# Kernel tuning notes

Measured on AMD Instinct MI355X. Metric: run time of the kernel, lower is better.

The kernel has to match this reference:

```python
import jax, jax.numpy as jnp
import numpy as np

N = 20000      # nodes (single node type)
E = 320000     # edges per relation (avg degree 16)
R = 3          # relations / edge types
L = 3          # layers
H = 4          # heads
D = 64         # dim per head (hid_size // n_heads)
IN = 256       # in_size == hid_size
OUT = 128      # out_size
NEG_SLOPE = 0.2


def setup_inputs() -> dict:
    key = jax.random.key(0)
    ks = jax.random.split(key, 8)
    x = jax.random.normal(ks[0], (N, IN), jnp.float32)
    edge_src = jax.random.randint(ks[1], (R, E), 0, N, dtype=jnp.int32)
    edge_dst = jax.random.randint(ks[2], (R, E), 0, N, dtype=jnp.int32)
    W = jax.random.normal(ks[3], (L, R, IN, H * D), jnp.float32) * (1.0 / np.sqrt(IN))
    attn_l = jax.random.normal(ks[4], (L, R, H, D), jnp.float32) * 0.1
    attn_r = jax.random.normal(ks[5], (L, R, H, D), jnp.float32) * 0.1
    bias = jnp.zeros((L, R, H * D), jnp.float32)
    fc_w = jax.random.normal(ks[6], (IN, OUT), jnp.float32) * (1.0 / np.sqrt(IN))
    fc_b = jnp.zeros((OUT,), jnp.float32)
    return dict(x=x, edge_src=edge_src, edge_dst=edge_dst, W=W,
                attn_l=attn_l, attn_r=attn_r, bias=bias, fc_w=fc_w, fc_b=fc_b)


def _gat_conv(h, src, dst, W_r, al, ar, b_r):
    # h: [N, IN] -> feat: [N, H, D]
    feat = (h @ W_r).reshape(N, H, D)
    el = jnp.sum(feat * al, axis=-1)                      # [N, H]
    er = jnp.sum(feat * ar, axis=-1)                      # [N, H]
    e = jax.nn.leaky_relu(el[src] + er[dst], NEG_SLOPE)   # [E, H]
    # segment softmax over incoming edges of each dst node, per head
    m = jax.ops.segment_max(e, dst, num_segments=N)       # [N, H]
    a = jnp.exp(e - m[dst])
    s = jax.ops.segment_sum(a, dst, num_segments=N)       # [N, H]
    alpha = a / s[dst]                                    # [E, H]
    # weighted scatter-add of source features: [N, H, D]
    out = jax.ops.segment_sum(alpha[:, :, None] * feat[src], dst, num_segments=N)
    return out + b_r.reshape(1, H, D)


def reference(x, edge_src, edge_dst, W, attn_l, attn_r, bias, fc_w, fc_b):
    h = x
    for l in range(L):
        acc = jnp.zeros((N, H, D), h.dtype)
        for r in range(R):  # sum-aggregate across relations (HeteroGraphConv aggregate='sum')
            acc = acc + _gat_conv(h, edge_src[r], edge_dst[r],
                                  W[l, r], attn_l[l, r], attn_r[l, r], bias[l, r])
        h = acc.reshape(N, H * D)
        if l != L - 1:
            h = jax.nn.relu(h)  # dropout = identity in eval
    return h @ fc_w + fc_b  # [N, OUT]
```

## Files before the change

kernel.cpp:

```cpp
#include <hip/hip_runtime.h>
#include <math.h>

#define NN 20000
#define NN_PAD 20096
#define EE 320000
#define RR 3
#define LL 3
#define HH 4
#define DD 64
#define CDIM 256
#define OUTD 128
#define NEG 0.2f

typedef float f32x4 __attribute__((ext_vector_type(4)));
typedef short sh8 __attribute__((ext_vector_type(8)));

__device__ __forceinline__ ushort f2bf(float f) {
    union { float f; uint u; } v; v.f = f;
    uint r = (v.u + 0x7FFF + ((v.u >> 16) & 1)) >> 16;
    return (ushort)r;
}
__device__ __forceinline__ float bf2f(ushort u) {
    union { uint u; float f; } v; v.u = ((uint)u) << 16;
    return v.f;
}
__device__ __forceinline__ float bflo(uint p) { return bf2f((ushort)(p & 0xffff)); }
__device__ __forceinline__ float bfhi(uint p) { return bf2f((ushort)(p >> 16)); }

__device__ __forceinline__ void glds16(const ushort* g, ushort* l) {
    __builtin_amdgcn_global_load_lds(
        (const __attribute__((address_space(1))) void*)g,
        (__attribute__((address_space(3))) void*)l, 16, 0, 0);
}


__global__ void count_deg(const int* __restrict__ edge_dst, int* __restrict__ deg) {
    int i = blockIdx.x * blockDim.x + threadIdx.x;
    if (i >= RR * EE) return;
    int r = i / EE;
    atomicAdd(&deg[r * NN + edge_dst[i]], 1);
}

__global__ __launch_bounds__(1024) void scan_kernel(
    const int* __restrict__ deg, int* __restrict__ row_ptr, int* __restrict__ cursor) {
    int r = blockIdx.x;
    const int* d = deg + r * NN;
    int* rp = row_ptr + r * (NN + 1);
    int* cur = cursor + r * (NN + 1);
    __shared__ int wsum[16];
    int lane = threadIdx.x & 63, wv = threadIdx.x >> 6;
    if (threadIdx.x == 0) { rp[0] = 0; cur[0] = 0; }
    int carry = 0;
    for (int base = 0; base < NN; base += 1024) {
        int i = base + threadIdx.x;
        int v = (i < NN) ? d[i] : 0;
        int s = v;
        #pragma unroll
        for (int off = 1; off < 64; off <<= 1) {
            int n = __shfl_up(s, off, 64);
            if (lane >= off) s += n;
        }
        if (lane == 63) wsum[wv] = s;
        __syncthreads();
        if (wv == 0) {
            int ws = (lane < 16) ? wsum[lane] : 0;
            #pragma unroll
            for (int off = 1; off < 16; off <<= 1) {
                int n = __shfl_up(ws, off, 64);
                if (lane >= off) ws += n;
            }
            if (lane < 16) wsum[lane] = ws;
        }
        __syncthreads();
        int incl = carry + (wv ? wsum[wv - 1] : 0) + s;
        if (i < NN) { rp[i + 1] = incl; cur[i + 1] = incl; }
        carry += wsum[15];
        __syncthreads();
    }
}

__global__ void fill_csr(const int* __restrict__ edge_src, const int* __restrict__ edge_dst,
                         int* __restrict__ cursor, int* __restrict__ csr_src) {
    int i = blockIdx.x * blockDim.x + threadIdx.x;
    if (i >= RR * EE) return;
    int r = i / EE;
    int dst = edge_dst[i];
    int pos = atomicAdd(&cursor[r * (NN + 1) + dst], 1);
    csr_src[r * EE + pos] = edge_src[i];
}


__global__ void cvt_bf16x4(const float* __restrict__ in, ushort* __restrict__ out, int n4) {
    int i = blockIdx.x * blockDim.x + threadIdx.x;
    if (i >= n4) return;
    float4 v = *(const float4*)(in + (size_t)i * 4);
    ushort4 o;
    o.x = f2bf(v.x); o.y = f2bf(v.y); o.z = f2bf(v.z); o.w = f2bf(v.w);
    *(ushort4*)(out + (size_t)i * 4) = o;
}

__global__ void prep_all(const float* __restrict__ W, const float* __restrict__ fc_w,
                         ushort* __restrict__ Wt, ushort* __restrict__ fct) {
    __shared__ float tile[32][33];
    int z = blockIdx.z;
    const float* src;
    ushort* dst;
    int N;
    if (z < LL * RR) {
        src = W + (size_t)z * CDIM * CDIM;
        dst = Wt + (size_t)z * CDIM * CDIM;
        N = CDIM;
    } else {
        src = fc_w;
        dst = fct;
        N = OUTD;
    }
    int kb = blockIdx.x * 32, nb = blockIdx.y * 32;
    if (nb >= N) return;
    for (int yy = threadIdx.y; yy < 32; yy += 8)
        tile[yy][threadIdx.x] = src[(size_t)(kb + yy) * N + nb + threadIdx.x];
    __syncthreads();
    for (int yy = threadIdx.y; yy < 32; yy += 8)
        dst[(size_t)(nb + yy) * CDIM + kb + threadIdx.x] = f2bf(tile[threadIdx.x][yy]);
}


#define TM 128
#define TN 128
#define TK 32

__global__ __launch_bounds__(256) void gemm_bf16(
    const ushort* __restrict__ A, const ushort* __restrict__ Bt0, void* __restrict__ C0,
    int M, int K, int Ncol, long strideB, long strideC,
    const float* __restrict__ bias, int out_fp32,
    const float* __restrict__ al_all, const float* __restrict__ ar_all,
    float* __restrict__ el_all, float* __restrict__ er_all) {
    __shared__ alignas(16) ushort As[TM * 32];
    __shared__ alignas(16) ushort Bs[TN * 32];
    const ushort* Bt = Bt0 + (size_t)blockIdx.z * strideB;
    int m0 = blockIdx.x * TM, n0 = blockIdx.y * TN;
    int t = threadIdx.x;
    int wave = t >> 6, lane = t & 63;
    int q = lane >> 4, l16 = lane & 15;
    int wrow = (wave >> 1) * 64, wcol = (wave & 1) * 64;

    int sw = (q ^ ((l16 >> 1) & 3)) * 8;
    int a_off[4], b_off[4];
    #pragma unroll
    for (int i = 0; i < 4; i++) {
        a_off[i] = (wrow + i * 16 + l16) * 32 + sw;
        b_off[i] = (wcol + i * 16 + l16) * 32 + sw;
    }
    int row_a = t >> 2;
    int ch_a  = ((t & 3) ^ ((row_a >> 1) & 3)) * 8;

    f32x4 acc[4][4];
    #pragma unroll
    for (int i = 0; i < 4; i++)
        #pragma unroll
        for (int j = 0; j < 4; j++)
            #pragma unroll
            for (int k = 0; k < 4; k++) acc[i][j][k] = 0.f;

    for (int k0 = 0; k0 < K; k0 += TK) {
        #pragma unroll
        for (int s = 0; s < 2; s++) {
            int qid = t + s * 256;
            int row = row_a + s * 64;
            glds16(A + (size_t)(m0 + row) * K + k0 + ch_a, As + qid * 8);
        }
        #pragma unroll
        for (int s = 0; s < 2; s++) {
            int qid = t + s * 256;
            int row = row_a + s * 64;
            glds16(Bt + (size_t)(n0 + row) * K + k0 + ch_a, Bs + qid * 8);
        }
        __syncthreads();
        sh8 af[4], bfr[4];
        #pragma unroll
        for (int i = 0; i < 4; i++) af[i] = *(const sh8*)(As + a_off[i]);
        #pragma unroll
        for (int j = 0; j < 4; j++) bfr[j] = *(const sh8*)(Bs + b_off[j]);
        #pragma unroll
        for (int i = 0; i < 4; i++)
            #pragma unroll
            for (int j = 0; j < 4; j++)
                acc[i][j] = __builtin_amdgcn_mfma_f32_16x16x32_bf16(af[i], bfr[j], acc[i][j], 0, 0, 0);
        __syncthreads();
    }

    if (out_fp32) {
        float* C = (float*)C0 + (size_t)blockIdx.z * strideC;
        #pragma unroll
        for (int i = 0; i < 4; i++) {
            #pragma unroll
            for (int reg = 0; reg < 4; reg++) {
                int row = m0 + wrow + i * 16 + q * 4 + reg;
                if (row >= M) continue;
                #pragma unroll
                for (int j = 0; j < 4; j++) {
                    int col = n0 + wcol + j * 16 + l16;
                    float v = acc[i][j][reg];
                    if (bias) v += bias[col];
                    C[(size_t)row * Ncol + col] = v;
                }
            }
        }
    } else {
        ushort* C = (ushort*)C0 + (size_t)blockIdx.z * strideC;
        #pragma unroll
        for (int i = 0; i < 4; i++) {
            #pragma unroll
            for (int reg = 0; reg < 4; reg++) {
                int row = m0 + wrow + i * 16 + q * 4 + reg;
                if (row >= M) continue;
                #pragma unroll
                for (int j = 0; j < 4; j++) {
                    int col = n0 + wcol + j * 16 + l16;
                    C[(size_t)row * Ncol + col] = f2bf(acc[i][j][reg]);
                }
            }
        }
    }

    if (el_all) {
        const float* al = al_all + (size_t)blockIdx.z * CDIM;
        const float* ar = ar_all + (size_t)blockIdx.z * CDIM;
        float* elp = el_all + (size_t)blockIdx.z * NN * HH;
        float* erp = er_all + (size_t)blockIdx.z * NN * HH;
        int head = (n0 + wcol) >> 6;
        float alj[4], arj[4];
        #pragma unroll
        for (int j = 0; j < 4; j++) {
            int gcol = n0 + wcol + j * 16 + l16;
            alj[j] = al[gcol];
            arj[j] = ar[gcol];
        }
        #pragma unroll
        for (int i = 0; i < 4; i++) {
            #pragma unroll
            for (int reg = 0; reg < 4; reg++) {
                int row = m0 + wrow + i * 16 + q * 4 + reg;
                float pl = 0.f, pr = 0.f;
                #pragma unroll
                for (int j = 0; j < 4; j++) {
                    pl = fmaf(acc[i][j][reg], alj[j], pl);
                    pr = fmaf(acc[i][j][reg], arj[j], pr);
                }
                #pragma unroll
                for (int m = 1; m < 16; m <<= 1) {
                    pl += __shfl_xor(pl, m, 64);
                    pr += __shfl_xor(pr, m, 64);
                }
                if (l16 == 0 && row < M) {
                    elp[(size_t)row * HH + head] = pl;
                    erp[(size_t)row * HH + head] = pr;
                }
            }
        }
    }
}

__global__ __launch_bounds__(256) void aggregate_fused(
    const ushort* __restrict__ feat16, const float* __restrict__ el,
    const float* __restrict__ er, const int* __restrict__ row_ptr,
    const int* __restrict__ csr_src, const float* __restrict__ bias,
    ushort* __restrict__ hout, int relu) {
    int wv = threadIdx.x >> 6, lane = threadIdx.x & 63;
    int node = blockIdx.x * 4 + wv;
    if (node >= NN) return;
    int c0 = lane * 4;
    int h = lane >> 4;
    float t0 = 0.f, t1 = 0.f, t2 = 0.f, t3 = 0.f;
    #pragma unroll
    for (int r = 0; r < RR; r++) {
        const int* rp = row_ptr + r * (NN + 1);
        int beg = rp[node], end = rp[node + 1];
        const ushort* fr = feat16 + (size_t)r * NN * CDIM;
        const float* elr = el + (size_t)r * NN * HH;
        float ern = er[((size_t)r * NN + node) * HH + h];
        const int* cs = csr_src + (size_t)r * EE;
        float p0 = 0.f, p1 = 0.f, p2 = 0.f, p3 = 0.f, ssum = 0.f;
        int e = beg;
        for (; e + 4 <= end; e += 4) {
            int s0 = cs[e], s1 = cs[e + 1], s2 = cs[e + 2], s3 = cs[e + 3];
            float x0 = elr[s0 * HH + h];
            float x1 = elr[s1 * HH + h];
            float x2 = elr[s2 * HH + h];
            float x3 = elr[s3 * HH + h];
            uint2 f0 = *(const uint2*)(fr + (size_t)s0 * CDIM + c0);
            uint2 f1 = *(const uint2*)(fr + (size_t)s1 * CDIM + c0);
            uint2 f2 = *(const uint2*)(fr + (size_t)s2 * CDIM + c0);
            uint2 f3 = *(const uint2*)(fr + (size_t)s3 * CDIM + c0);
            x0 += ern; x1 += ern; x2 += ern; x3 += ern;
            x0 = x0 > 0.f ? x0 : NEG * x0;
            x1 = x1 > 0.f ? x1 : NEG * x1;
            x2 = x2 > 0.f ? x2 : NEG * x2;
            x3 = x3 > 0.f ? x3 : NEG * x3;
            float a0 = __expf(x0), a1 = __expf(x1), a2 = __expf(x2), a3 = __expf(x3);
            ssum += a0 + a1 + a2 + a3;
            p0 = fmaf(a0, bflo(f0.x), p0); p1 = fmaf(a0, bfhi(f0.x), p1);
            p2 = fmaf(a0, bflo(f0.y), p2); p3 = fmaf(a0, bfhi(f0.y), p3);
            p0 = fmaf(a1, bflo(f1.x), p0); p1 = fmaf(a1, bfhi(f1.x), p1);
            p2 = fmaf(a1, bflo(f1.y), p2); p3 = fmaf(a1, bfhi(f1.y), p3);
            p0 = fmaf(a2, bflo(f2.x), p0); p1 = fmaf(a2, bfhi(f2.x), p1);
            p2 = fmaf(a2, bflo(f2.y), p2); p3 = fmaf(a2, bfhi(f2.y), p3);
            p0 = fmaf(a3, bflo(f3.x), p0); p1 = fmaf(a3, bfhi(f3.x), p1);
            p2 = fmaf(a3, bflo(f3.y), p2); p3 = fmaf(a3, bfhi(f3.y), p3);
        }
        for (; e < end; e++) {
            int s = cs[e];
            float x = elr[s * HH + h] + ern;
            x = x > 0.f ? x : NEG * x;
            float a = __expf(x);
            uint2 f = *(const uint2*)(fr + (size_t)s * CDIM + c0);
            ssum += a;
            p0 = fmaf(a, bflo(f.x), p0); p1 = fmaf(a, bfhi(f.x), p1);
            p2 = fmaf(a, bflo(f.y), p2); p3 = fmaf(a, bfhi(f.y), p3);
        }
        float is = (end > beg) ? 1.f / ssum : 0.f;
        t0 += p0 * is + bias[r * CDIM + c0];
        t1 += p1 * is + bias[r * CDIM + c0 + 1];
        t2 += p2 * is + bias[r * CDIM + c0 + 2];
        t3 += p3 * is + bias[r * CDIM + c0 + 3];
    }
    if (relu) {
        t0 = fmaxf(t0, 0.f); t1 = fmaxf(t1, 0.f);
        t2 = fmaxf(t2, 0.f); t3 = fmaxf(t3, 0.f);
    }
    uint2 o;
    o.x = (uint)f2bf(t0) | ((uint)f2bf(t1) << 16);
    o.y = (uint)f2bf(t2) | ((uint)f2bf(t3) << 16);
    *(uint2*)(hout + (size_t)node * CDIM + c0) = o;
}


extern "C" void kernel_launch(void* const* d_in, const int* in_sizes, int n_in,
                              void* d_out, int out_size, void* d_ws, size_t ws_size,
                              hipStream_t stream) {
    const float* x        = (const float*)d_in[0];
    const int*   edge_src = (const int*)d_in[1];
    const int*   edge_dst = (const int*)d_in[2];
    const float* W        = (const float*)d_in[3];
    const float* attn_l   = (const float*)d_in[4];
    const float* attn_r   = (const float*)d_in[5];
    const float* bias     = (const float*)d_in[6];
    const float* fc_w     = (const float*)d_in[7];
    const float* fc_b     = (const float*)d_in[8];
    float* out = (float*)d_out;

    char* ws = (char*)d_ws;
    size_t off = 0;
    auto alloc = [&](size_t bytes) {
        void* p = ws + off;
        off = (off + bytes + 255) & ~(size_t)255;
        return p;
    };
    ushort* x16    = (ushort*)alloc((size_t)NN_PAD * CDIM * 2);
    ushort* h16    = (ushort*)alloc((size_t)NN_PAD * CDIM * 2);
    ushort* feat16 = (ushort*)alloc((size_t)RR * NN * CDIM * 2);
    ushort* Wt16   = (ushort*)alloc((size_t)LL * RR * CDIM * CDIM * 2);
    ushort* fct16  = (ushort*)alloc((size_t)OUTD * CDIM * 2);
    float* el      = (float*)alloc((size_t)RR * NN * HH * 4);
    float* er      = (float*)alloc((size_t)RR * NN * HH * 4);
    int* row_ptr   = (int*)alloc((size_t)RR * (NN + 1) * 4);
    int* cursor    = (int*)alloc((size_t)RR * (NN + 1) * 4);
    int* csr_src   = (int*)alloc((size_t)RR * EE * 4);
    int* deg       = (int*)alloc((size_t)RR * NN * 4);

    hipMemsetAsync(deg, 0, (size_t)RR * NN * 4, stream);
    count_deg<<<dim3((RR * EE + 255) / 256), dim3(256), 0, stream>>>(edge_dst, deg);
    scan_kernel<<<dim3(RR), dim3(1024), 0, stream>>>(deg, row_ptr, cursor);
    fill_csr<<<dim3((RR * EE + 255) / 256), dim3(256), 0, stream>>>(
        edge_src, edge_dst, cursor, csr_src);

    cvt_bf16x4<<<dim3((NN * CDIM / 4 + 255) / 256), dim3(256), 0, stream>>>(x, x16, NN * CDIM / 4);
    prep_all<<<dim3(CDIM / 32, CDIM / 32, LL * RR + 1), dim3(32, 8), 0, stream>>>(
        W, fc_w, Wt16, fct16);

    const ushort* hin = x16;
    for (int l = 0; l < LL; l++) {
        const ushort* Wl = Wt16 + (size_t)l * RR * CDIM * CDIM;
        dim3 g(NN_PAD / TM, CDIM / TN, RR);
        gemm_bf16<<<g, dim3(256), 0, stream>>>(hin, Wl, feat16, NN, CDIM, CDIM,
                                               (long)CDIM * CDIM, (long)NN * CDIM, nullptr, 0,
                                               attn_l + (size_t)l * RR * CDIM,
                                               attn_r + (size_t)l * RR * CDIM, el, er);
        aggregate_fused<<<dim3(NN / 4), dim3(256), 0, stream>>>(
            feat16, el, er, row_ptr, csr_src, bias + (size_t)l * RR * CDIM,
            h16, (l != LL - 1) ? 1 : 0);
        hin = h16;
    }
    dim3 gf(NN_PAD / TM, OUTD / TN, 1);
    gemm_bf16<<<gf, dim3(256), 0, stream>>>(h16, fct16, out, NN, CDIM, OUTD,
                                            0, 0, fc_b, 1, nullptr, nullptr, nullptr, nullptr);
}
```

Before: 513.4 us.

## Add full-width 128x256 feature GEMM with K=64 stages, specialize final GEMM

Adds a dedicated per-layer feature GEMM in which each block computes a full 256-column output tile (128x256) with K-steps of 64. Each A row-block is loaded once instead of twice across column tiles, and there are half as many K-loop barriers. The el/er attention epilogue now handles two heads per wave. The generic GEMM is cut down to the fp32+bias output path used by the final FC layer. The trade-off is more LDS (48KB) and a larger accumulator register footprint (128 floats per thread), which may lower occupancy, and the grid has half as many blocks (471).

```diff
diff --git a/kernel.cpp b/kernel.cpp
--- a/kernel.cpp
+++ b/kernel.cpp
@@ -125,19 +125,132 @@
 }
 
 
+__global__ __launch_bounds__(256) void gemm_feat(
+    const ushort* __restrict__ A, const ushort* __restrict__ Wt0, ushort* __restrict__ C0,
+    const float* __restrict__ al_all, const float* __restrict__ ar_all,
+    float* __restrict__ el_all, float* __restrict__ er_all) {
+    __shared__ alignas(16) ushort As[128 * 64];
+    __shared__ alignas(16) ushort Bs[256 * 64];
+    const int K = CDIM;
+    const ushort* Bt = Wt0 + (size_t)blockIdx.z * CDIM * CDIM;
+    int m0 = blockIdx.x * 128;
+    int t = threadIdx.x;
+    int wave = t >> 6, lane = t & 63;
+    int q = lane >> 4, l16 = lane & 15;
+    int wrow = (wave >> 1) * 64, wcol = (wave & 1) * 128;
+
+    f32x4 acc[4][8];
+    #pragma unroll
+    for (int i = 0; i < 4; i++)
+        #pragma unroll
+        for (int j = 0; j < 8; j++)
+            #pragma unroll
+            for (int k = 0; k < 4; k++) acc[i][j][k] = 0.f;
+
+    int srow = t >> 3, sch = t & 7;
+
+    for (int k0 = 0; k0 < K; k0 += 64) {
+        #pragma unroll
+        for (int s = 0; s < 4; s++) {
+            int row = srow + s * 32;
+            int gch = (sch ^ (row & 7)) * 8;
+            glds16(A + (size_t)(m0 + row) * K + k0 + gch, As + (t + s * 256) * 8);
+        }
+        #pragma unroll
+        for (int s = 0; s < 8; s++) {
+            int row = srow + s * 32;
+            int gch = (sch ^ (row & 7)) * 8;
+            glds16(Bt + (size_t)row * K + k0 + gch, Bs + (t + s * 256) * 8);
+        }
+        __syncthreads();
+        #pragma unroll
+        for (int s = 0; s < 2; s++) {
+            int csw = ((s * 4 + q) ^ (l16 & 7)) * 8;
+            sh8 af[4], bfr[8];
+            #pragma unroll
+            for (int i = 0; i < 4; i++)
+                af[i] = *(const sh8*)(As + (wrow + i * 16 + l16) * 64 + csw);
+            #pragma unroll
+            for (int j = 0; j < 8; j++)
+                bfr[j] = *(const sh8*)(Bs + (wcol + j * 16 + l16) * 64 + csw);
+            #pragma unroll
+            for (int i = 0; i < 4; i++)
+                #pragma unroll
+                for (int j = 0; j < 8; j++)
+                    acc[i][j] = __builtin_amdgcn_mfma_f32_16x16x32_bf16(af[i], bfr[j], acc[i][j], 0, 0, 0);
+        }
+        __syncthreads();
+    }
+
+    ushort* C = C0 + (size_t)blockIdx.z * NN * CDIM;
+    #pragma unroll
+    for (int i = 0; i < 4; i++) {
+        #pragma unroll
+        for (int reg = 0; reg < 4; reg++) {
+            int row = m0 + wrow + i * 16 + q * 4 + reg;
+            if (row >= NN) continue;
+            #pragma unroll
+            for (int j = 0; j < 8; j++) {
+                int col = wcol + j * 16 + l16;
+                C[(size_t)row * CDIM + col] = f2bf(acc[i][j][reg]);
+            }
+        }
+    }
+
+    {
+        const float* al = al_all + (size_t)blockIdx.z * CDIM;
+        const float* ar = ar_all + (size_t)blockIdx.z * CDIM;
+        float* elp = el_all + (size_t)blockIdx.z * NN * HH;
+        float* erp = er_all + (size_t)blockIdx.z * NN * HH;
+        int head0 = wcol >> 6;
+        float alj[8], arj[8];
+        #pragma unroll
+        for (int j = 0; j < 8; j++) {
+            int gcol = wcol + j * 16 + l16;
+            alj[j] = al[gcol];
+            arj[j] = ar[gcol];
+        }
+        #pragma unroll
+        for (int i = 0; i < 4; i++) {
+            #pragma unroll
+            for (int reg = 0; reg < 4; reg++) {
+                int row = m0 + wrow + i * 16 + q * 4 + reg;
+                float pl0 = 0.f, pr0 = 0.f, pl1 = 0.f, pr1 = 0.f;
+                #pragma unroll
+                for (int j = 0; j < 4; j++) {
+                    pl0 = fmaf(acc[i][j][reg], alj[j], pl0);
+                    pr0 = fmaf(acc[i][j][reg], arj[j], pr0);
+                    pl1 = fmaf(acc[i][j + 4][reg], alj[j + 4], pl1);
+                    pr1 = fmaf(acc[i][j + 4][reg], arj[j + 4], pr1);
+                }
+                #pragma unroll
+                for (int m = 1; m < 16; m <<= 1) {
+                    pl0 += __shfl_xor(pl0, m, 64);
+                    pr0 += __shfl_xor(pr0, m, 64);
+                    pl1 += __shfl_xor(pl1, m, 64);
+                    pr1 += __shfl_xor(pr1, m, 64);
+                }
+                if (l16 == 0 && row < NN) {
+                    elp[(size_t)row * HH + head0] = pl0;
+                    erp[(size_t)row * HH + head0] = pr0;
+                    elp[(size_t)row * HH + head0 + 1] = pl1;
+                    erp[(size_t)row * HH + head0 + 1] = pr1;
+                }
+            }
+        }
+    }
+}
+
+
 #define TM 128
 #define TN 128
 #define TK 32
 
 __global__ __launch_bounds__(256) void gemm_bf16(
-    const ushort* __restrict__ A, const ushort* __restrict__ Bt0, void* __restrict__ C0,
-    int M, int K, int Ncol, long strideB, long strideC,
-    const float* __restrict__ bias, int out_fp32,
-    const float* __restrict__ al_all, const float* __restrict__ ar_all,
-    float* __restrict__ el_all, float* __restrict__ er_all) {
+    const ushort* __restrict__ A, const ushort* __restrict__ Bt, float* __restrict__ C,
+    int M, int K, int Ncol, const float* __restrict__ bias) {
     __shared__ alignas(16) ushort As[TM * 32];
     __shared__ alignas(16) ushort Bs[TN * 32];
-    const ushort* Bt = Bt0 + (size_t)blockIdx.z * strideB;
     int m0 = blockIdx.x * TM, n0 = blockIdx.y * TN;
     int t = threadIdx.x;
     int wave = t >> 6, lane = t & 63;
@@ -189,73 +302,16 @@
         __syncthreads();
     }
 
-    if (out_fp32) {
-        float* C = (float*)C0 + (size_t)blockIdx.z * strideC;
-        #pragma unroll
-        for (int i = 0; i < 4; i++) {
-            #pragma unroll
-            for (int reg = 0; reg < 4; reg++) {
-                int row = m0 + wrow + i * 16 + q * 4 + reg;
-                if (row >= M) continue;
-                #pragma unroll
-                for (int j = 0; j < 4; j++) {
-                    int col = n0 + wcol + j * 16 + l16;
-                    float v = acc[i][j][reg];
-                    if (bias) v += bias[col];
-                    C[(size_t)row * Ncol + col] = v;
-                }
-            }
-        }
-    } else {
-        ushort* C = (ushort*)C0 + (size_t)blockIdx.z * strideC;
-        #pragma unroll
-        for (int i = 0; i < 4; i++) {
-            #pragma unroll
-            for (int reg = 0; reg < 4; reg++) {
-                int row = m0 + wrow + i * 16 + q * 4 + reg;
-                if (row >= M) continue;
-                #pragma unroll
-                for (int j = 0; j < 4; j++) {
-                    int col = n0 + wcol + j * 16 + l16;
-                    C[(size_t)row * Ncol + col] = f2bf(acc[i][j][reg]);
-                }
-            }
-        }
-    }
-
-    if (el_all) {
-        const float* al = al_all + (size_t)blockIdx.z * CDIM;
-        const float* ar = ar_all + (size_t)blockIdx.z * CDIM;
-        float* elp = el_all + (size_t)blockIdx.z * NN * HH;
-        float* erp = er_all + (size_t)blockIdx.z * NN * HH;
-        int head = (n0 + wcol) >> 6;
-        float alj[4], arj[4];
-        #pragma unroll
-        for (int j = 0; j < 4; j++) {
-            int gcol = n0 + wcol + j * 16 + l16;
-            alj[j] = al[gcol];
-            arj[j] = ar[gcol];
-        }
-        #pragma unroll
-        for (int i = 0; i < 4; i++) {
-            #pragma unroll
-            for (int reg = 0; reg < 4; reg++) {
-                int row = m0 + wrow + i * 16 + q * 4 + reg;
-                float pl = 0.f, pr = 0.f;
-                #pragma unroll
-                for (int j = 0; j < 4; j++) {
-                    pl = fmaf(acc[i][j][reg], alj[j], pl);
-                    pr = fmaf(acc[i][j][reg], arj[j], pr);
-                }
-                #pragma unroll
-                for (int m = 1; m < 16; m <<= 1) {
-                    pl += __shfl_xor(pl, m, 64);
-                    pr += __shfl_xor(pr, m, 64);
-                }
-                if (l16 == 0 && row < M) {
-                    elp[(size_t)row * HH + head] = pl;
-                    erp[(size_t)row * HH + head] = pr;
-                }
+    #pragma unroll
+    for (int i = 0; i < 4; i++) {
+        #pragma unroll
+        for (int reg = 0; reg < 4; reg++) {
+            int row = m0 + wrow + i * 16 + q * 4 + reg;
+            if (row >= M) continue;
+            #pragma unroll
+            for (int j = 0; j < 4; j++) {
+                int col = n0 + wcol + j * 16 + l16;
+                C[(size_t)row * Ncol + col] = acc[i][j][reg] + bias[col];
             }
         }
     }
@@ -381,17 +437,14 @@
     const ushort* hin = x16;
     for (int l = 0; l < LL; l++) {
         const ushort* Wl = Wt16 + (size_t)l * RR * CDIM * CDIM;
-        dim3 g(NN_PAD / TM, CDIM / TN, RR);
-        gemm_bf16<<<g, dim3(256), 0, stream>>>(hin, Wl, feat16, NN, CDIM, CDIM,
-                                               (long)CDIM * CDIM, (long)NN * CDIM, nullptr, 0,
-                                               attn_l + (size_t)l * RR * CDIM,
-                                               attn_r + (size_t)l * RR * CDIM, el, er);
+        gemm_feat<<<dim3(NN_PAD / 128, 1, RR), dim3(256), 0, stream>>>(
+            hin, Wl, feat16,
+            attn_l + (size_t)l * RR * CDIM, attn_r + (size_t)l * RR * CDIM, el, er);
         aggregate_fused<<<dim3(NN / 4), dim3(256), 0, stream>>>(
             feat16, el, er, row_ptr, csr_src, bias + (size_t)l * RR * CDIM,
             h16, (l != LL - 1) ? 1 : 0);
         hin = h16;
     }
-    dim3 gf(NN_PAD / TM, OUTD / TN, 1);
-    gemm_bf16<<<gf, dim3(256), 0, stream>>>(h16, fct16, out, NN, CDIM, OUTD,
-                                            0, 0, fc_b, 1, nullptr, nullptr, nullptr, nullptr);
-}
+    gemm_bf16<<<dim3(NN_PAD / TM, OUTD / TN), dim3(256), 0, stream>>>(
+        h16, fct16, out, NN, CDIM, OUTD, fc_b);
+}
```

After: 518.6 us. No clear change (+1.0%).

## Fuse CSR build and bf16 prep into one cooperative persistent kernel

Applied to the files above, without the earlier changes.

Replaces the memset, degree count, scan, CSR fill, input conversion and weight transpose kernels with a single cooperative kernel that uses grid-wide syncs between phases. This removes five launch boundaries and lets independent conversion work share a launch with the memset. The scan now runs with 256 threads per relation instead of 1024, so that serial phase becomes longer. The grid syncs also add cost, and the kernel is limited to 1024 blocks.

```diff
diff --git a/kernel.cpp b/kernel.cpp
--- a/kernel.cpp
+++ b/kernel.cpp
@@ -1,5 +1,8 @@
 #include <hip/hip_runtime.h>
+#include <hip/hip_cooperative_groups.h>
 #include <math.h>
+
+namespace cg = cooperative_groups;
 
 #define NN 20000
 #define NN_PAD 20096
@@ -34,94 +37,92 @@
 }
 
 
-__global__ void count_deg(const int* __restrict__ edge_dst, int* __restrict__ deg) {
-    int i = blockIdx.x * blockDim.x + threadIdx.x;
-    if (i >= RR * EE) return;
-    int r = i / EE;
-    atomicAdd(&deg[r * NN + edge_dst[i]], 1);
-}
-
-__global__ __launch_bounds__(1024) void scan_kernel(
-    const int* __restrict__ deg, int* __restrict__ row_ptr, int* __restrict__ cursor) {
-    int r = blockIdx.x;
-    const int* d = deg + r * NN;
-    int* rp = row_ptr + r * (NN + 1);
-    int* cur = cursor + r * (NN + 1);
-    __shared__ int wsum[16];
-    int lane = threadIdx.x & 63, wv = threadIdx.x >> 6;
-    if (threadIdx.x == 0) { rp[0] = 0; cur[0] = 0; }
-    int carry = 0;
-    for (int base = 0; base < NN; base += 1024) {
-        int i = base + threadIdx.x;
-        int v = (i < NN) ? d[i] : 0;
-        int s = v;
-        #pragma unroll
-        for (int off = 1; off < 64; off <<= 1) {
-            int n = __shfl_up(s, off, 64);
-            if (lane >= off) s += n;
-        }
-        if (lane == 63) wsum[wv] = s;
-        __syncthreads();
-        if (wv == 0) {
-            int ws = (lane < 16) ? wsum[lane] : 0;
-            #pragma unroll
-            for (int off = 1; off < 16; off <<= 1) {
-                int n = __shfl_up(ws, off, 64);
-                if (lane >= off) ws += n;
-            }
-            if (lane < 16) wsum[lane] = ws;
-        }
-        __syncthreads();
-        int incl = carry + (wv ? wsum[wv - 1] : 0) + s;
-        if (i < NN) { rp[i + 1] = incl; cur[i + 1] = incl; }
-        carry += wsum[15];
-        __syncthreads();
-    }
-}
-
-__global__ void fill_csr(const int* __restrict__ edge_src, const int* __restrict__ edge_dst,
-                         int* __restrict__ cursor, int* __restrict__ csr_src) {
-    int i = blockIdx.x * blockDim.x + threadIdx.x;
-    if (i >= RR * EE) return;
-    int r = i / EE;
-    int dst = edge_dst[i];
-    int pos = atomicAdd(&cursor[r * (NN + 1) + dst], 1);
-    csr_src[r * EE + pos] = edge_src[i];
-}
-
-
-__global__ void cvt_bf16x4(const float* __restrict__ in, ushort* __restrict__ out, int n4) {
-    int i = blockIdx.x * blockDim.x + threadIdx.x;
-    if (i >= n4) return;
-    float4 v = *(const float4*)(in + (size_t)i * 4);
-    ushort4 o;
-    o.x = f2bf(v.x); o.y = f2bf(v.y); o.z = f2bf(v.z); o.w = f2bf(v.w);
-    *(ushort4*)(out + (size_t)i * 4) = o;
-}
-
-__global__ void prep_all(const float* __restrict__ W, const float* __restrict__ fc_w,
-                         ushort* __restrict__ Wt, ushort* __restrict__ fct) {
+__global__ __launch_bounds__(256) void build_all(
+    const float* __restrict__ x, const float* __restrict__ W,
+    const float* __restrict__ fc_w,
+    const int* __restrict__ edge_src, const int* __restrict__ edge_dst,
+    ushort* __restrict__ x16, ushort* __restrict__ Wt, ushort* __restrict__ fct,
+    int* __restrict__ deg, int* __restrict__ row_ptr,
+    int* __restrict__ cursor, int* __restrict__ csr_src) {
+    cg::grid_group grid = cg::this_grid();
+    int nb = gridDim.x, bid = blockIdx.x, t = threadIdx.x;
+    int gid = bid * 256 + t, gsz = nb * 256;
     __shared__ float tile[32][33];
-    int z = blockIdx.z;
-    const float* src;
-    ushort* dst;
-    int N;
-    if (z < LL * RR) {
-        src = W + (size_t)z * CDIM * CDIM;
-        dst = Wt + (size_t)z * CDIM * CDIM;
-        N = CDIM;
-    } else {
-        src = fc_w;
-        dst = fct;
-        N = OUTD;
-    }
-    int kb = blockIdx.x * 32, nb = blockIdx.y * 32;
-    if (nb >= N) return;
-    for (int yy = threadIdx.y; yy < 32; yy += 8)
-        tile[yy][threadIdx.x] = src[(size_t)(kb + yy) * N + nb + threadIdx.x];
-    __syncthreads();
-    for (int yy = threadIdx.y; yy < 32; yy += 8)
-        dst[(size_t)(nb + yy) * CDIM + kb + threadIdx.x] = f2bf(tile[threadIdx.x][yy]);
+    __shared__ int wsum[4];
+
+    for (int i = gid; i < RR * NN; i += gsz) deg[i] = 0;
+    for (int i = gid; i < NN * CDIM / 4; i += gsz) {
+        float4 v = *(const float4*)(x + (size_t)i * 4);
+        ushort4 o;
+        o.x = f2bf(v.x); o.y = f2bf(v.y); o.z = f2bf(v.z); o.w = f2bf(v.w);
+        *(ushort4*)(x16 + (size_t)i * 4) = o;
+    }
+    {
+        int tjobs = LL * RR * 64 + (CDIM / 32) * (OUTD / 32);
+        int tx = t & 31, ty = t >> 5;
+        for (int job = bid; job < tjobs; job += nb) {
+            const float* src; ushort* dst; int N, kb, nbv;
+            if (job < LL * RR * 64) {
+                int z = job >> 6, tj = job & 63;
+                src = W + (size_t)z * CDIM * CDIM;
+                dst = Wt + (size_t)z * CDIM * CDIM;
+                N = CDIM; kb = (tj >> 3) * 32; nbv = (tj & 7) * 32;
+            } else {
+                int tj = job - LL * RR * 64;
+                src = fc_w; dst = fct; N = OUTD;
+                kb = (tj >> 2) * 32; nbv = (tj & 3) * 32;
+            }
+            __syncthreads();
+            for (int yy = ty; yy < 32; yy += 8)
+                tile[yy][tx] = src[(size_t)(kb + yy) * N + nbv + tx];
+            __syncthreads();
+            for (int yy = ty; yy < 32; yy += 8)
+                dst[(size_t)(nbv + yy) * CDIM + kb + tx] = f2bf(tile[tx][yy]);
+        }
+    }
+    grid.sync();
+
+    for (int i = gid; i < RR * EE; i += gsz) {
+        int r = i / EE;
+        atomicAdd(&deg[r * NN + edge_dst[i]], 1);
+    }
+    grid.sync();
+
+    if (bid < RR) {
+        int r = bid;
+        const int* d = deg + r * NN;
+        int* rp = row_ptr + r * (NN + 1);
+        int* cur = cursor + r * (NN + 1);
+        int lane = t & 63, wv = t >> 6;
+        if (t == 0) { rp[0] = 0; cur[0] = 0; }
+        int carry = 0;
+        for (int base = 0; base < NN; base += 256) {
+            int i = base + t;
+            int v = (i < NN) ? d[i] : 0;
+            int s = v;
+            #pragma unroll
+            for (int off2 = 1; off2 < 64; off2 <<= 1) {
+                int n = __shfl_up(s, off2, 64);
+                if (lane >= off2) s += n;
+            }
+            if (lane == 63) wsum[wv] = s;
+            __syncthreads();
+            int wadd = 0;
+            for (int w = 0; w < wv; w++) wadd += wsum[w];
+            int incl = carry + wadd + s;
+            if (i < NN) { rp[i + 1] = incl; cur[i + 1] = incl; }
+            carry += wsum[0] + wsum[1] + wsum[2] + wsum[3];
+            __syncthreads();
+        }
+    }
+    grid.sync();
+
+    for (int i = gid; i < RR * EE; i += gsz) {
+        int r = i / EE;
+        int dst = edge_dst[i];
+        int pos = atomicAdd(&cursor[r * (NN + 1) + dst], 1);
+        csr_src[r * EE + pos] = edge_src[i];
+    }
 }
 
 
@@ -368,15 +369,16 @@
     int* csr_src   = (int*)alloc((size_t)RR * EE * 4);
     int* deg       = (int*)alloc((size_t)RR * NN * 4);
 
-    hipMemsetAsync(deg, 0, (size_t)RR * NN * 4, stream);
-    count_deg<<<dim3((RR * EE + 255) / 256), dim3(256), 0, stream>>>(edge_dst, deg);
-    scan_kernel<<<dim3(RR), dim3(1024), 0, stream>>>(deg, row_ptr, cursor);
-    fill_csr<<<dim3((RR * EE + 255) / 256), dim3(256), 0, stream>>>(
-        edge_src, edge_dst, cursor, csr_src);
-
-    cvt_bf16x4<<<dim3((NN * CDIM / 4 + 255) / 256), dim3(256), 0, stream>>>(x, x16, NN * CDIM / 4);
-    prep_all<<<dim3(CDIM / 32, CDIM / 32, LL * RR + 1), dim3(32, 8), 0, stream>>>(
-        W, fc_w, Wt16, fct16);
+    {
+        void* args[] = {
+            (void*)&x, (void*)&W, (void*)&fc_w,
+            (void*)&edge_src, (void*)&edge_dst,
+            (void*)&x16, (void*)&Wt16, (void*)&fct16,
+            (void*)&deg, (void*)&row_ptr, (void*)&cursor, (void*)&csr_src
+        };
+        hipLaunchCooperativeKernel((const void*)build_all, dim3(1024), dim3(256),
+                                   args, 0, stream);
+    }
 
     const ushort* hin = x16;
     for (int l = 0; l < LL; l++) {
```

Measured after the change: 896.6 us. 74.6% more time.
